# Optimization experiments

Hardware: AMD Instinct MI355X
Metric: run time of the kernel (lower is better)

The kernel has to match this reference:

```python
import jax, jax.numpy as jnp
import numpy as np

EPS = 1e-5
TOP_K = 2


def setup_inputs() -> dict:
    key = jax.random.key(0)
    ks = jax.random.split(key, 8)
    B, T, D, E, F = 4, 2048, 1024, 8, 4096
    s_in = 1.0 / np.sqrt(D)
    s_ff = 1.0 / np.sqrt(F)
    return {
        "hidden_states": jax.random.normal(ks[0], (B, T, D), jnp.float32),
        "input_tensor": jax.random.normal(ks[1], (B, T, D), jnp.float32),
        "gate_w": jax.random.normal(ks[2], (D, E), jnp.float32) * s_in,
        "gate_b": jnp.zeros((E,), jnp.float32),
        "w1": jax.random.normal(ks[3], (E, D, F), jnp.float32) * s_in,
        "b1": jnp.zeros((E, F), jnp.float32),
        "w2": jax.random.normal(ks[4], (E, F, D), jnp.float32) * s_ff,
        "b2": jnp.zeros((E, D), jnp.float32),
        "gamma": jnp.ones((D,), jnp.float32),
        "beta": jnp.zeros((D,), jnp.float32),
    }


def _layer_norm(x, gamma, beta):
    mu = jnp.mean(x, axis=-1, keepdims=True)
    var = jnp.mean(jnp.square(x - mu), axis=-1, keepdims=True)
    return (x - mu) * jax.lax.rsqrt(var + EPS) * gamma + beta


def reference(hidden_states, input_tensor, gate_w, gate_b, w1, b1, w2, b2, gamma, beta):
    E = gate_b.shape[0]
    # Router: softmax over experts, then top-k gate values/indices.
    gate_logits = jnp.einsum("btd,de->bte", hidden_states, gate_w) + gate_b
    gate_probs = jax.nn.softmax(gate_logits, axis=-1)
    topk_gates, topk_idx = jax.lax.top_k(gate_probs, TOP_K)  # [B,T,K]
    # Combine weights per expert: sum of top-k gate values routed to expert e.
    combine_w = jnp.sum(
        jax.nn.one_hot(topk_idx, E, dtype=hidden_states.dtype)
        * topk_gates[..., None],
        axis=-2,
    )  # [B,T,E]
    # Dispatch/combine: weighted sum of expert FFN outputs (loop over small fixed E).
    expert_outputs = jnp.zeros_like(hidden_states)
    for e in range(E):
        h = jax.nn.gelu(jnp.einsum("btd,df->btf", hidden_states, w1[e]) + b1[e])
        y = jnp.einsum("btf,fd->btd", h, w2[e]) + b2[e]
        expert_outputs = expert_outputs + combine_w[..., e:e + 1] * y
    # Dropout is identity in eval mode.
    return _layer_norm(expert_outputs + input_tensor, gamma, beta)
```

## Files before the change

### kernel.cpp

```cpp
#include <hip/hip_runtime.h>

#define TOKENS 8192
#define DIM 1024
#define NEXP 8
#define FDIM 4096

typedef __bf16 bf16x8 __attribute__((ext_vector_type(8)));
typedef float f32x4 __attribute__((ext_vector_type(4)));
typedef float f32x16 __attribute__((ext_vector_type(16)));

__device__ __forceinline__ unsigned short f2bf(float f) {
  unsigned u = __builtin_bit_cast(unsigned, f);
  u += 0x7fffu + ((u >> 16) & 1u);
  return (unsigned short)(u >> 16);
}

__device__ __forceinline__ float bf2f(unsigned short s) {
  unsigned u = (unsigned)s << 16;
  return __builtin_bit_cast(float, u);
}

__device__ __forceinline__ void gload16(const void* g, void* l) {
  __builtin_amdgcn_global_load_lds(
      (const __attribute__((address_space(1))) unsigned int*)g,
      (__attribute__((address_space(3))) unsigned int*)l, 16, 0, 0);
}

__global__ void zero_counts_kernel(int* counts) {
  if (threadIdx.x < NEXP) counts[threadIdx.x] = 0;
}

__global__ void scan_kernel(const int* counts, int* offs, int* nchk,
                            int* chunks0, int* chunks1) {
  if (threadIdx.x == 0) {
    int s = 0;
    for (int e = 0; e < NEXP; ++e) { offs[e] = s; s += counts[e]; }
    offs[NEXP] = s;
    int nc0 = 0, nc1 = 0;
    for (int e = 0; e < NEXP; ++e) {
      const int mt = (counts[e] + 127) >> 7;
      for (int mc = 0; mc < mt; mc += 4) {
        for (int n4 = 0; n4 < 32; n4 += 4)
          chunks0[nc0++] = (e << 16) | (mc << 8) | n4;
        for (int n4 = 0; n4 < 8; n4 += 4)
          chunks1[nc1++] = (e << 16) | (mc << 8) | n4;
      }
    }
    nchk[0] = nc0;
    nchk[1] = nc1;
  }
}

__global__ void router_kernel(const float* __restrict__ hs,
                              const float* __restrict__ gw,
                              const float* __restrict__ gb,
                              int* __restrict__ counts,
                              int* __restrict__ tok_idx,
                              float* __restrict__ tok_w,
                              unsigned int* __restrict__ slotinfo,
                              unsigned short* __restrict__ hs_bf) {
  const int lane = threadIdx.x & 63;
  const int wid = threadIdx.x >> 6;
  const int t = blockIdx.x * 4 + wid;
  const float* row = hs + (size_t)t * DIM;

  float x[16];
  const float4* r4 = (const float4*)(row + lane * 16);
#pragma unroll
  for (int i = 0; i < 4; ++i) {
    float4 v = r4[i];
    x[i * 4 + 0] = v.x; x[i * 4 + 1] = v.y; x[i * 4 + 2] = v.z; x[i * 4 + 3] = v.w;
  }

  float acc[8];
#pragma unroll
  for (int e = 0; e < 8; ++e) acc[e] = 0.f;
#pragma unroll
  for (int i = 0; i < 16; ++i) {
    const int d = lane * 16 + i;
    const float4* g4 = (const float4*)(gw + (size_t)d * 8);
    float4 g0 = g4[0], g1 = g4[1];
    const float xv = x[i];
    acc[0] += xv * g0.x; acc[1] += xv * g0.y; acc[2] += xv * g0.z; acc[3] += xv * g0.w;
    acc[4] += xv * g1.x; acc[5] += xv * g1.y; acc[6] += xv * g1.z; acc[7] += xv * g1.w;
  }
#pragma unroll
  for (int sh = 1; sh < 64; sh <<= 1) {
#pragma unroll
    for (int e = 0; e < 8; ++e) acc[e] += __shfl_xor(acc[e], sh, 64);
  }
#pragma unroll
  for (int e = 0; e < 8; ++e) acc[e] += gb[e];

  float mx = acc[0];
#pragma unroll
  for (int e = 1; e < 8; ++e) mx = fmaxf(mx, acc[e]);
  float p[8];
  float sum = 0.f;
#pragma unroll
  for (int e = 0; e < 8; ++e) { p[e] = __expf(acc[e] - mx); sum += p[e]; }
  const float inv = 1.0f / sum;

  int i0 = 0; float b0 = p[0];
#pragma unroll
  for (int e = 1; e < 8; ++e) if (p[e] > b0) { b0 = p[e]; i0 = e; }
  int i1 = -1; float b1v = -1.f;
#pragma unroll
  for (int e = 0; e < 8; ++e) if (e != i0 && p[e] > b1v) { b1v = p[e]; i1 = e; }

  if (lane == 0) {
    int pos0 = atomicAdd(&counts[i0], 1);
    tok_idx[i0 * TOKENS + pos0] = t;
    tok_w[i0 * TOKENS + pos0] = b0 * inv;
    int pos1 = atomicAdd(&counts[i1], 1);
    tok_idx[i1 * TOKENS + pos1] = t;
    tok_w[i1 * TOKENS + pos1] = b1v * inv;
    slotinfo[t] = ((unsigned)i0 << 29) | ((unsigned)pos0 << 16) |
                  ((unsigned)i1 << 13) | (unsigned)pos1;
  }

  unsigned short us[16];
#pragma unroll
  for (int i = 0; i < 16; ++i) us[i] = f2bf(x[i]);
  uint4 o0, o1;
  o0.x = (unsigned)us[0] | ((unsigned)us[1] << 16);
  o0.y = (unsigned)us[2] | ((unsigned)us[3] << 16);
  o0.z = (unsigned)us[4] | ((unsigned)us[5] << 16);
  o0.w = (unsigned)us[6] | ((unsigned)us[7] << 16);
  o1.x = (unsigned)us[8] | ((unsigned)us[9] << 16);
  o1.y = (unsigned)us[10] | ((unsigned)us[11] << 16);
  o1.z = (unsigned)us[12] | ((unsigned)us[13] << 16);
  o1.w = (unsigned)us[14] | ((unsigned)us[15] << 16);
  uint4* dst = (uint4*)(hs_bf + (size_t)t * DIM + lane * 16);
  dst[0] = o0;
  dst[1] = o1;
}

__global__ void cast_transpose_all(const float* __restrict__ w1,
                                   unsigned short* __restrict__ w1t,
                                   const float* __restrict__ w2,
                                   unsigned short* __restrict__ w2t) {
  __shared__ float tile[64][65];
  const int L = blockIdx.x;
  const float* src;
  unsigned short* dstp;
  int R, C, bi;
  if (L < 8192) { src = w1; dstp = w1t; R = DIM;  C = FDIM; bi = L; }
  else          { src = w2; dstp = w2t; R = FDIM; C = DIM;  bi = L - 8192; }
  const int nx = C >> 6;
  const int e = bi >> 10;
  const int w = bi & 1023;
  const int by = w / nx, bx = w % nx;
  const int r0 = by * 64, c0 = bx * 64;
  const float* s = src + (size_t)e * R * C;
  unsigned int* d = (unsigned int*)(dstp + (size_t)e * R * C);

#pragma unroll
  for (int i = 0; i < 16; ++i) {
    const int idx = threadIdx.x + i * 256;
    const int r = idx >> 6;
    const int c = idx & 63;
    tile[r][c] = s[(size_t)(r0 + r) * C + (c0 + c)];
  }
  __syncthreads();
#pragma unroll
  for (int i = 0; i < 8; ++i) {
    const int idx = threadIdx.x + i * 256;
    const int c = idx >> 5;
    const int r = (idx & 31) * 2;
    unsigned pk = (unsigned)f2bf(tile[r][c]) | ((unsigned)f2bf(tile[r + 1][c]) << 16);
    d[((size_t)(c0 + c) * R + (r0 + r)) >> 1] = pk;
  }
}

template<int MODE, int K, int N>
__global__ __launch_bounds__(256, 4)
void moe_gemm(const unsigned short* __restrict__ Abase,
              const unsigned short* __restrict__ Bbase,
              const float* __restrict__ bias,
              const int* __restrict__ counts,
              const int* __restrict__ offs,
              const int* __restrict__ tok_idx,
              const int* __restrict__ chunktab,
              const int* __restrict__ nchk,
              unsigned short* __restrict__ dst) {
  constexpr int NS = K / 64;
  __shared__ __align__(16) unsigned char sm[32768];

  const int L = blockIdx.x;
  const int xk = L & 7;
  const int tt = L >> 3;
  const int g = (tt >> 4) * 8 + xk;
  if (g >= nchk[MODE]) return;
  const int within = tt & 15;
  const int cd = chunktab[g];
  const int e = cd >> 16;
  const int cnt = counts[e];
  const int m0 = (((cd >> 8) & 255) + (within >> 2)) * 128;
  if (m0 >= cnt) return;
  const int n0 = ((cd & 255) + (within & 3)) * 128;
  const int goff = offs[e];

  const int tid = threadIdx.x;
  const int lane = tid & 63;
  const int wid = tid >> 6;
  const int wm = wid >> 1;
  const int wn = wid & 1;
  const int l31 = lane & 31;
  const int lh = lane >> 5;

  const int trow = tid >> 2;
  const int tswz = (tid & 3) ^ ((trow >> 1) & 3);
  const unsigned char* Bexp = (const unsigned char*)(Bbase + (size_t)e * K * N);

  int gA0 = m0 + trow;      if (gA0 > cnt - 1) gA0 = cnt - 1;
  int gA1 = m0 + trow + 64; if (gA1 > cnt - 1) gA1 = cnt - 1;
  size_t rowA0, rowA1;
  if (MODE == 0) {
    rowA0 = (size_t)tok_idx[e * TOKENS + gA0] * K;
    rowA1 = (size_t)tok_idx[e * TOKENS + gA1] * K;
  } else {
    rowA0 = (size_t)(goff + gA0) * K;
    rowA1 = (size_t)(goff + gA1) * K;
  }
  const unsigned char* pA0 = (const unsigned char*)(Abase + rowA0) + tswz * 16;
  const unsigned char* pA1 = (const unsigned char*)(Abase + rowA1) + tswz * 16;
  const unsigned char* pB0 = Bexp + (size_t)(n0 + trow) * (K * 2) + tswz * 16;
  const unsigned char* pB1 = Bexp + (size_t)(n0 + trow + 64) * (K * 2) + tswz * 16;

  const int sw = (l31 >> 1) & 3;
  const int cE = lh ^ sw;
  const int aB0 = wm * 4096 + l31 * 64 + cE * 16;
  const int aB1 = wm * 4096 + l31 * 64 + (cE ^ 2) * 16;
  const int bB0 = 16384 + wn * 4096 + l31 * 64 + cE * 16;
  const int bB1 = 16384 + wn * 4096 + l31 * 64 + (cE ^ 2) * 16;
  const unsigned char* smc = (const unsigned char*)sm;
  unsigned char* smw = (unsigned char*)sm + tid * 16;

  f32x16 acc[2][2];
#pragma unroll
  for (int mb = 0; mb < 2; ++mb)
#pragma unroll
    for (int nb = 0; nb < 2; ++nb)
#pragma unroll
      for (int r = 0; r < 16; ++r) acc[mb][nb][r] = 0.f;

#pragma unroll 1
  for (int st = 0; st < NS; ++st) {
    gload16(pA0, smw);
    gload16(pA1, smw + 4096);
    gload16(pA0 + 64, smw + 8192);
    gload16(pA1 + 64, smw + 12288);
    gload16(pB0, smw + 16384);
    gload16(pB1, smw + 20480);
    gload16(pB0 + 64, smw + 24576);
    gload16(pB1 + 64, smw + 28672);
    pA0 += 128; pA1 += 128; pB0 += 128; pB1 += 128;
    __syncthreads();
#pragma unroll
    for (int kq = 0; kq < 4; ++kq) {
      const int sb = (kq >> 1) * 8192;
      const int ap = (kq & 1) ? aB1 : aB0;
      const int bp = (kq & 1) ? bB1 : bB0;
      bf16x8 a0 = *(const bf16x8*)(smc + sb + ap);
      bf16x8 a1 = *(const bf16x8*)(smc + sb + ap + 2048);
      bf16x8 b0 = *(const bf16x8*)(smc + sb + bp);
      bf16x8 b1 = *(const bf16x8*)(smc + sb + bp + 2048);
      acc[0][0] = __builtin_amdgcn_mfma_f32_32x32x16_bf16(a0, b0, acc[0][0], 0, 0, 0);
      acc[0][1] = __builtin_amdgcn_mfma_f32_32x32x16_bf16(a0, b1, acc[0][1], 0, 0, 0);
      acc[1][0] = __builtin_amdgcn_mfma_f32_32x32x16_bf16(a1, b0, acc[1][0], 0, 0, 0);
      acc[1][1] = __builtin_amdgcn_mfma_f32_32x32x16_bf16(a1, b1, acc[1][1], 0, 0, 0);
    }
    __syncthreads();
  }

#pragma unroll
  for (int nb = 0; nb < 2; ++nb) {
    const int fcol = n0 + wn * 64 + nb * 32 + l31;
    const float bv = bias[e * N + fcol];
#pragma unroll
    for (int mb = 0; mb < 2; ++mb) {
#pragma unroll
      for (int r = 0; r < 16; ++r) {
        const int ml = wm * 64 + mb * 32 + (r & 3) + 8 * (r >> 2) + 4 * lh;
        const int gm = m0 + ml;
        if (gm < cnt) {
          float v = acc[mb][nb][r] + bv;
          if (MODE == 0) {
            const float u = 0.7978845608028654f * (v + 0.044715f * v * v * v);
            const float th = 1.0f - 2.0f / (1.0f + __expf(2.0f * u));
            v = 0.5f * v * (1.0f + th);
          }
          dst[(size_t)(goff + gm) * N + fcol] = f2bf(v);
        }
      }
    }
  }
}

__global__ void ln_combine_kernel(const unsigned short* __restrict__ y_buf,
                                  const float* __restrict__ in_t,
                                  const int* __restrict__ offs,
                                  const unsigned int* __restrict__ slotinfo,
                                  const float* __restrict__ tok_w,
                                  const float* __restrict__ gamma,
                                  const float* __restrict__ beta,
                                  float* __restrict__ out) {
  const int lane = threadIdx.x & 63;
  const int wid = threadIdx.x >> 6;
  const int t = blockIdx.x * 4 + wid;

  const unsigned s = slotinfo[t];
  const int e0 = s >> 29, p0 = (s >> 16) & 8191;
  const int e1 = (s >> 13) & 7, p1 = s & 8191;
  const float w0 = tok_w[e0 * TOKENS + p0];
  const float w1 = tok_w[e1 * TOKENS + p1];
  const size_t r0 = (size_t)(offs[e0] + p0) * DIM;
  const size_t r1 = (size_t)(offs[e1] + p1) * DIM;

  float v[16];
  {
    const float4* i4 = (const float4*)(in_t + (size_t)t * DIM + lane * 16);
    const uint4* y0 = (const uint4*)(y_buf + r0 + lane * 16);
    const uint4* y1 = (const uint4*)(y_buf + r1 + lane * 16);
#pragma unroll
    for (int i = 0; i < 4; ++i) {
      float4 a = i4[i];
      v[i * 4 + 0] = a.x; v[i * 4 + 1] = a.y; v[i * 4 + 2] = a.z; v[i * 4 + 3] = a.w;
    }
#pragma unroll
    for (int i = 0; i < 2; ++i) {
      uint4 u0 = y0[i];
      uint4 u1 = y1[i];
      const unsigned uw0[4] = {u0.x, u0.y, u0.z, u0.w};
      const unsigned uw1[4] = {u1.x, u1.y, u1.z, u1.w};
#pragma unroll
      for (int k = 0; k < 4; ++k) {
        const int base = i * 8 + k * 2;
        v[base + 0] += w0 * bf2f((unsigned short)(uw0[k] & 0xffff)) +
                       w1 * bf2f((unsigned short)(uw1[k] & 0xffff));
        v[base + 1] += w0 * bf2f((unsigned short)(uw0[k] >> 16)) +
                       w1 * bf2f((unsigned short)(uw1[k] >> 16));
      }
    }
  }

  float sum = 0.f, s2 = 0.f;
#pragma unroll
  for (int i = 0; i < 16; ++i) { sum += v[i]; s2 += v[i] * v[i]; }
#pragma unroll
  for (int sh = 1; sh < 64; sh <<= 1) {
    sum += __shfl_xor(sum, sh, 64);
    s2 += __shfl_xor(s2, sh, 64);
  }
  const float mu = sum * (1.0f / DIM);
  const float var = s2 * (1.0f / DIM) - mu * mu;
  const float rs = rsqrtf(var + 1e-5f);

  float4* w4 = (float4*)(out + (size_t)t * DIM + lane * 16);
#pragma unroll
  for (int i = 0; i < 4; ++i) {
    const int d = lane * 16 + i * 4;
    float4 gg = *(const float4*)(gamma + d);
    float4 bb = *(const float4*)(beta + d);
    float4 o;
    o.x = (v[i * 4 + 0] - mu) * rs * gg.x + bb.x;
    o.y = (v[i * 4 + 1] - mu) * rs * gg.y + bb.y;
    o.z = (v[i * 4 + 2] - mu) * rs * gg.z + bb.z;
    o.w = (v[i * 4 + 3] - mu) * rs * gg.w + bb.w;
    w4[i] = o;
  }
}

extern "C" void kernel_launch(void* const* d_in, const int* in_sizes, int n_in,
                              void* d_out, int out_size, void* d_ws, size_t ws_size,
                              hipStream_t stream) {
  const float* hs    = (const float*)d_in[0];
  const float* in_t  = (const float*)d_in[1];
  const float* gw    = (const float*)d_in[2];
  const float* gb    = (const float*)d_in[3];
  const float* w1    = (const float*)d_in[4];
  const float* b1    = (const float*)d_in[5];
  const float* w2    = (const float*)d_in[6];
  const float* b2    = (const float*)d_in[7];
  const float* gamma = (const float*)d_in[8];
  const float* beta  = (const float*)d_in[9];
  float* out = (float*)d_out;
  char* ws = (char*)d_ws;

  int* counts            = (int*)(ws + 0);
  int* offs              = (int*)(ws + 256);
  unsigned int* slotinfo = (unsigned int*)(ws + 512);
  int* nchk              = (int*)(ws + 33280);
  int* chunks0           = (int*)(ws + 33536);
  int* chunks1           = (int*)(ws + 35072);
  int* tok_idx           = (int*)(ws + 66048);
  float* tok_w           = (float*)(ws + 328192);
  unsigned short* hs_bf  = (unsigned short*)(ws + 590336);
  unsigned short* w1t    = (unsigned short*)(ws + 17367552);
  unsigned short* w2t    = (unsigned short*)(ws + 84476416);
  unsigned short* h_buf  = (unsigned short*)(ws + 151585280);
  unsigned short* y_buf  = (unsigned short*)(ws + 590336);

  zero_counts_kernel<<<1, 64, 0, stream>>>(counts);
  router_kernel<<<TOKENS / 4, 256, 0, stream>>>(hs, gw, gb, counts, tok_idx, tok_w,
                                                slotinfo, hs_bf);
  scan_kernel<<<1, 64, 0, stream>>>(counts, offs, nchk, chunks0, chunks1);
  cast_transpose_all<<<16384, 256, 0, stream>>>(w1, w1t, w2, w2t);
  moe_gemm<0, DIM, FDIM><<<6144, 256, 0, stream>>>(
      hs_bf, w1t, b1, counts, offs, tok_idx, chunks0, nchk, h_buf);
  moe_gemm<1, FDIM, DIM><<<2048, 256, 0, stream>>>(
      h_buf, w2t, b2, counts, offs, tok_idx, chunks1, nchk, y_buf);
  ln_combine_kernel<<<TOKENS / 4, 256, 0, stream>>>(y_buf, in_t, offs, slotinfo,
                                                    tok_w, gamma, beta, out);
}
```

Baseline: 736.8 us.

## Double-buffer LDS tiles in MoE GEMM to overlap global loads with MFMA

Shrinks the per-stage K slice from 64 to 32 and splits the 32KB LDS into two 16KB buffers. The next stage's tiles are prefetched with global_load_lds while MFMAs run on the current buffer, using explicit vmcnt waits and raw barriers in place of __syncthreads. The aim is to hide global memory latency behind compute. In exchange the loop runs twice as many iterations, each with two barriers, and correctness depends on the hand-written waitcnt ordering.

```diff
diff --git a/kernel.cpp b/kernel.cpp
--- a/kernel.cpp
+++ b/kernel.cpp
@@ -184,7 +184,7 @@
               const int* __restrict__ chunktab,
               const int* __restrict__ nchk,
               unsigned short* __restrict__ dst) {
-  constexpr int NS = K / 64;
+  constexpr int NS = K / 32;
   __shared__ __align__(16) unsigned char sm[32768];
 
   const int L = blockIdx.x;
@@ -230,10 +230,8 @@
 
   const int sw = (l31 >> 1) & 3;
   const int cE = lh ^ sw;
-  const int aB0 = wm * 4096 + l31 * 64 + cE * 16;
-  const int aB1 = wm * 4096 + l31 * 64 + (cE ^ 2) * 16;
-  const int bB0 = 16384 + wn * 4096 + l31 * 64 + cE * 16;
-  const int bB1 = 16384 + wn * 4096 + l31 * 64 + (cE ^ 2) * 16;
+  const int aB = wm * 4096 + l31 * 64 + cE * 16;
+  const int bB = 8192 + wn * 4096 + l31 * 64 + cE * 16;
   const unsigned char* smc = (const unsigned char*)sm;
   unsigned char* smw = (unsigned char*)sm + tid * 16;
 
@@ -245,33 +243,43 @@
 #pragma unroll
       for (int r = 0; r < 16; ++r) acc[mb][nb][r] = 0.f;
 
+  gload16(pA0, smw);
+  gload16(pA1, smw + 4096);
+  gload16(pB0, smw + 8192);
+  gload16(pB1, smw + 12288);
+  pA0 += 64; pA1 += 64; pB0 += 64; pB1 += 64;
+
 #pragma unroll 1
   for (int st = 0; st < NS; ++st) {
-    gload16(pA0, smw);
-    gload16(pA1, smw + 4096);
-    gload16(pA0 + 64, smw + 8192);
-    gload16(pA1 + 64, smw + 12288);
-    gload16(pB0, smw + 16384);
-    gload16(pB1, smw + 20480);
-    gload16(pB0 + 64, smw + 24576);
-    gload16(pB1 + 64, smw + 28672);
-    pA0 += 128; pA1 += 128; pB0 += 128; pB1 += 128;
-    __syncthreads();
-#pragma unroll
-    for (int kq = 0; kq < 4; ++kq) {
-      const int sb = (kq >> 1) * 8192;
-      const int ap = (kq & 1) ? aB1 : aB0;
-      const int bp = (kq & 1) ? bB1 : bB0;
-      bf16x8 a0 = *(const bf16x8*)(smc + sb + ap);
-      bf16x8 a1 = *(const bf16x8*)(smc + sb + ap + 2048);
-      bf16x8 b0 = *(const bf16x8*)(smc + sb + bp);
-      bf16x8 b1 = *(const bf16x8*)(smc + sb + bp + 2048);
+    const int cs = (st & 1) << 14;
+    const int ns = ((st + 1) & 1) << 14;
+    if (st < NS - 1) {
+      gload16(pA0, smw + ns);
+      gload16(pA1, smw + ns + 4096);
+      gload16(pB0, smw + ns + 8192);
+      gload16(pB1, smw + ns + 12288);
+      pA0 += 64; pA1 += 64; pB0 += 64; pB1 += 64;
+      asm volatile("s_waitcnt vmcnt(4)" ::: "memory");
+    } else {
+      asm volatile("s_waitcnt vmcnt(0)" ::: "memory");
+    }
+    __builtin_amdgcn_s_barrier();
+    __builtin_amdgcn_sched_barrier(0);
+#pragma unroll
+    for (int kq = 0; kq < 2; ++kq) {
+      const int ko = kq << 5;
+      bf16x8 a0 = *(const bf16x8*)(smc + cs + (aB ^ ko));
+      bf16x8 a1 = *(const bf16x8*)(smc + cs + ((aB + 2048) ^ ko));
+      bf16x8 b0 = *(const bf16x8*)(smc + cs + (bB ^ ko));
+      bf16x8 b1 = *(const bf16x8*)(smc + cs + ((bB + 2048) ^ ko));
       acc[0][0] = __builtin_amdgcn_mfma_f32_32x32x16_bf16(a0, b0, acc[0][0], 0, 0, 0);
       acc[0][1] = __builtin_amdgcn_mfma_f32_32x32x16_bf16(a0, b1, acc[0][1], 0, 0, 0);
       acc[1][0] = __builtin_amdgcn_mfma_f32_32x32x16_bf16(a1, b0, acc[1][0], 0, 0, 0);
       acc[1][1] = __builtin_amdgcn_mfma_f32_32x32x16_bf16(a1, b1, acc[1][1], 0, 0, 0);
     }
-    __syncthreads();
+    __builtin_amdgcn_sched_barrier(0);
+    asm volatile("s_waitcnt lgkmcnt(0)" ::: "memory");
+    __builtin_amdgcn_s_barrier();
   }
 
 #pragma unroll
```

New measurement: 729.9 us. No clear change (-0.9%).
